# Kernel tuning notes

Hardware: AMD Instinct MI355X
Metric: run time of the kernel (lower is better)

## Reference

```python
import jax, jax.numpy as jnp
import numpy as np

B, DIM_IN, DIM_OUT = 2048, 4096, 4096


def setup_inputs() -> dict:
    key = jax.random.key(0)
    k1, k2, k3 = jax.random.split(key, 3)
    # binary input activations (0/1), stored as int32
    x = jax.random.randint(k1, (B, DIM_IN), 0, 2, dtype=jnp.int32)
    masks = jax.random.uniform(k2, (DIM_IN, DIM_OUT)) < 0.5
    # integer thresholds in [0, dim_in)
    thresholds = jax.random.randint(k3, (DIM_OUT,), 0, DIM_IN, dtype=jnp.int32)
    return {"x": x, "masks": masks, "thresholds": thresholds}


def reference(x, masks, thresholds):
    # Original: expand x to (B, dim_in, dim_out), XNOR with masks, sum over dim_in,
    # compare vs thresholds. XNOR(a,b) = a*b + (1-a)*(1-b), so the sum over dim_in
    # is two GEMMs -- never materialize the (B, dim_in, dim_out) tensor.
    xf = x.astype(jnp.float32)              # (B, dim_in), values in {0,1}
    mf = masks.astype(jnp.float32)          # (dim_in, dim_out)
    sums = xf @ mf + (1.0 - xf) @ (1.0 - mf)  # (B, dim_out), popcount of agreements
    return sums > thresholds.astype(jnp.float32)[None, :]  # (B, dim_out) bool
```

## Files before the change

### kernel.cpp

```cpp
#include <hip/hip_runtime.h>
#include <stdint.h>

#define BB    2048
#define DIN   4096
#define DOUT  4096


using v4i  = __attribute__((ext_vector_type(4)))  int;
using v16i = __attribute__((ext_vector_type(16))) int;

__device__ __forceinline__ void async_load16(const void* g, void* l) {
    __builtin_amdgcn_global_load_lds(
        (const __attribute__((address_space(1))) unsigned int*)g,
        (__attribute__((address_space(3))) unsigned int*)l,
        16, 0, 0);
}

__device__ __forceinline__ unsigned int to_pm1(unsigned int c) {
    return c + ((c ^ 0x01010101u) * 255u);
}

__global__ void pack_all(const int* __restrict__ x,
                         const void* __restrict__ mraw,
                         char* __restrict__ x8,
                         char* __restrict__ m8T) {
    const int tid = threadIdx.x;
    if (blockIdx.x < BB) {
        const int row = blockIdx.x;
        const int4* src = (const int4*)(x + (size_t)row * DIN);
        unsigned int* dst = (unsigned int*)(x8 + (size_t)row * DIN);
        #pragma unroll
        for (int q = 0; q < 4; ++q) {
            int4 v = src[q * 256 + tid];
            unsigned int t = (unsigned int)(v.x & 1) |
                             ((unsigned int)(v.y & 1) << 8) |
                             ((unsigned int)(v.z & 1) << 16) |
                             ((unsigned int)(v.w & 1) << 24);
            dst[q * 256 + tid] = to_pm1(t);
        }
    } else {
        const int bw = blockIdx.x - BB;
        const int n0 = (bw >> 4) * 64;
        const int k0 = (bw & 15) * 256;

        __shared__ unsigned int tl[64][68];

        const unsigned char* mb = (const unsigned char*)mraw;
        const unsigned int pv = *(const unsigned int*)(mb + (tid & 63) * 4);
        const bool isU8 = __any(pv > 1u);

        const int kq4  = tid >> 2;
        const int nq16 = (tid & 3) * 16;
        unsigned int b[4][4];
        if (isU8) {
            #pragma unroll
            for (int r = 0; r < 4; ++r) {
                uint4 v = *(const uint4*)(mb + (size_t)(k0 + kq4 * 4 + r) * DOUT
                                          + n0 + nq16);
                b[r][0] = v.x; b[r][1] = v.y; b[r][2] = v.z; b[r][3] = v.w;
            }
        } else {
            const int4* m32 = (const int4*)mraw;
            #pragma unroll
            for (int r = 0; r < 4; ++r)
                #pragma unroll
                for (int q = 0; q < 4; ++q) {
                    int4 v = m32[((size_t)(k0 + kq4 * 4 + r) * DOUT
                                  + n0 + nq16 + q * 4) >> 2];
                    b[r][q] = (unsigned int)(v.x & 1) |
                              ((unsigned int)(v.y & 1) << 8) |
                              ((unsigned int)(v.z & 1) << 16) |
                              ((unsigned int)(v.w & 1) << 24);
                }
        }
        #pragma unroll
        for (int w = 0; w < 4; ++w) {
            unsigned int a0 = b[0][w], a1 = b[1][w], a2 = b[2][w], a3 = b[3][w];
            unsigned int x0 = __builtin_amdgcn_perm(a1, a0, 0x05010400u);
            unsigned int x1 = __builtin_amdgcn_perm(a3, a2, 0x05010400u);
            unsigned int x2 = __builtin_amdgcn_perm(a1, a0, 0x07030602u);
            unsigned int x3 = __builtin_amdgcn_perm(a3, a2, 0x07030602u);
            unsigned int c0 = __builtin_amdgcn_perm(x1, x0, 0x05040100u);
            unsigned int c1 = __builtin_amdgcn_perm(x1, x0, 0x07060302u);
            unsigned int c2 = __builtin_amdgcn_perm(x3, x2, 0x05040100u);
            unsigned int c3 = __builtin_amdgcn_perm(x3, x2, 0x07060302u);
            tl[nq16 + w * 4 + 0][kq4] = to_pm1(c0);
            tl[nq16 + w * 4 + 1][kq4] = to_pm1(c1);
            tl[nq16 + w * 4 + 2][kq4] = to_pm1(c2);
            tl[nq16 + w * 4 + 3][kq4] = to_pm1(c3);
        }
        __syncthreads();

        const int nr = tid >> 2;
        const int c4 = tid & 3;
        #pragma unroll
        for (int q = 0; q < 4; ++q) {
            uint4 v = *(const uint4*)&tl[nr][4 * (c4 + 4 * q)];
            *(uint4*)(m8T + (size_t)(n0 + nr) * DIN + k0 + 16 * (c4 + 4 * q)) = v;
        }
    }
}

__global__ __launch_bounds__(512)
void bgemm(const char* __restrict__ x8,
           const char* __restrict__ m8T,
           const int* __restrict__ thr,
           int* __restrict__ out) {
    const int flat = blockIdx.x;
    const int xcd  = flat & 7;
    const int idx  = flat >> 3;
    const int bm   = (xcd & 1) * 4 + (idx & 3);
    const int bn   = (xcd >> 1) * 8 + (idx >> 2);
    const int b0   = bm * 256;
    const int o0   = bn * 128;

    const int tid  = threadIdx.x;
    const int lane = tid & 63;
    const int wv   = tid >> 6;
    const int im   = wv & 1;
    const int in_  = (wv >> 1) & 1;
    const int kh   = wv >> 2;
    const int wm   = im * 128;
    const int wn   = in_ * 64;
    const int l31  = lane & 31;
    const int lh   = lane >> 5;
    const int rsw  = l31 & 7;

    __shared__ __align__(16) char lds[3 * 49152];

    auto stage = [&](int c, int buf) {
        char* bufA = lds + buf * 49152;
        char* bufB = bufA + 32768;
        const int k0 = c * 128;
        const int r8 = lane >> 3;
        const int sl = lane & 7;
        #pragma unroll
        for (int h = 0; h < 4; ++h) {
            const int r0  = wv * 32 + h * 8;
            const int row = r0 + r8;
            const int g   = sl ^ (row & 7);
            async_load16(x8 + (size_t)(b0 + row) * DIN + k0 + g * 16,
                         bufA + r0 * 128 + lane * 16);
        }
        #pragma unroll
        for (int h = 0; h < 2; ++h) {
            const int r0  = wv * 16 + h * 8;
            const int row = r0 + r8;
            const int g   = sl ^ (row & 7);
            async_load16(m8T + (size_t)(o0 + row) * DIN + k0 + g * 16,
                         bufB + r0 * 128 + lane * 16);
        }
    };

    v16i acc[4][2];
    #pragma unroll
    for (int t = 0; t < 4; ++t)
        #pragma unroll
        for (int u = 0; u < 2; ++u)
            acc[t][u] = (v16i)(0);

    stage(0, 0);
    stage(1, 1);

    for (int c = 0; c < 32; ++c) {
        if (c < 31) asm volatile("s_waitcnt vmcnt(6)" ::: "memory");
        else        asm volatile("s_waitcnt vmcnt(0)" ::: "memory");
        __builtin_amdgcn_s_barrier();
        if (c < 30) stage(c + 2, (c + 2) % 3);

        const char* bufA = lds + (c % 3) * 49152;
        const char* bufB = bufA + 32768;
        #pragma unroll
        for (int ks = 0; ks < 2; ++ks) {
            const int slot = (((kh * 4 + ks * 2 + lh) ^ rsw)) * 16;
            v4i aF[4], bF[2];
            #pragma unroll
            for (int t = 0; t < 4; ++t)
                aF[t] = *(const v4i*)&bufA[(wm + t * 32 + l31) * 128 + slot];
            #pragma unroll
            for (int u = 0; u < 2; ++u)
                bF[u] = *(const v4i*)&bufB[(wn + u * 32 + l31) * 128 + slot];
            #pragma unroll
            for (int t = 0; t < 4; ++t)
                #pragma unroll
                for (int u = 0; u < 2; ++u)
                    acc[t][u] = __builtin_amdgcn_mfma_i32_32x32x32_i8(
                        aF[t], bF[u], acc[t][u], 0, 0, 0);
        }
    }
    __syncthreads();

    int* pool = (int*)lds;
    const int p = wv & 3;
    {
        const int give0 = kh ? 0 : 2;
        const int bw_ = p * 8192 + (kh ? 0 : 1) * 4096;
        #pragma unroll
        for (int tt = 0; tt < 2; ++tt) {
            const int t = give0 + tt;
            #pragma unroll
            for (int u = 0; u < 2; ++u)
                #pragma unroll
                for (int r = 0; r < 16; ++r) {
                    const int rowl = (r & 3) + 8 * (r >> 2) + 4 * lh;
                    pool[bw_ + (tt * 32 + rowl) * 64 + u * 32 + l31] = acc[t][u][r];
                }
        }
    }
    __syncthreads();
    const int keep0 = kh ? 2 : 0;
    const int br_ = p * 8192 + kh * 4096;
    #pragma unroll
    for (int tt = 0; tt < 2; ++tt) {
        const int t = keep0 + tt;
        #pragma unroll
        for (int u = 0; u < 2; ++u)
            #pragma unroll
            for (int r = 0; r < 16; ++r) {
                const int rowl = (r & 3) + 8 * (r >> 2) + 4 * lh;
                acc[t][u][r] += pool[br_ + (tt * 32 + rowl) * 64 + u * 32 + l31];
            }
    }

    #pragma unroll
    for (int u = 0; u < 2; ++u) {
        const int o   = o0 + wn + u * 32 + l31;
        const int lim = 2 * thr[o] - DIN;
        #pragma unroll
        for (int tt = 0; tt < 2; ++tt) {
            const int t = keep0 + tt;
            #pragma unroll
            for (int r = 0; r < 16; ++r) {
                const int rowl = (r & 3) + 8 * (r >> 2) + 4 * lh;
                const int b    = b0 + wm + kh * 64 + tt * 32 + rowl;
                out[(size_t)b * DOUT + o] = (acc[t][u][r] > lim) ? 1 : 0;
            }
        }
    }
}

extern "C" void kernel_launch(void* const* d_in, const int* in_sizes, int n_in,
                              void* d_out, int out_size, void* d_ws, size_t ws_size,
                              hipStream_t stream) {
    const int* x          = (const int*)d_in[0];
    const void* masks     = d_in[1];
    const int* thresholds = (const int*)d_in[2];
    int* out              = (int*)d_out;

    char* x8  = (char*)d_ws;
    char* m8T = (char*)d_ws + ((size_t)8 << 20);

    pack_all<<<BB + 1024, 256, 0, stream>>>(x, masks, x8, m8T);
    bgemm<<<256, 512, 0, stream>>>(x8, m8T, thresholds, out);
}
```

Before: 174.0 us.

## Pack operands into MFMA fragment-major layout for contiguous loads

The pack kernel now writes x and the transposed mask directly in a fragment-tiled layout: 32 rows by 32 k-bytes, each 1 KB block ordered the way a lane reads it. The GEMM stage loads each 1 KB fragment as one contiguous wave-wide async copy. LDS reads become lane*16 offsets with no XOR swizzle. This is meant to make global loads fully coalesced and to remove swizzle address math and LDS bank conflicts. The pack-side writes become more scattered, and the linear LDS reads may bring back bank conflicts.

```diff
diff --git a/kernel.cpp b/kernel.cpp
--- a/kernel.cpp
+++ b/kernel.cpp
@@ -22,13 +22,14 @@
 
 __global__ void pack_all(const int* __restrict__ x,
                          const void* __restrict__ mraw,
-                         char* __restrict__ x8,
-                         char* __restrict__ m8T) {
+                         char* __restrict__ x8f,
+                         char* __restrict__ m8Tf) {
     const int tid = threadIdx.x;
     if (blockIdx.x < BB) {
         const int row = blockIdx.x;
+        const int rb  = row >> 5;
+        const int rl  = row & 31;
         const int4* src = (const int4*)(x + (size_t)row * DIN);
-        unsigned int* dst = (unsigned int*)(x8 + (size_t)row * DIN);
         #pragma unroll
         for (int q = 0; q < 4; ++q) {
             int4 v = src[q * 256 + tid];
@@ -36,7 +37,10 @@
                              ((unsigned int)(v.y & 1) << 8) |
                              ((unsigned int)(v.z & 1) << 16) |
                              ((unsigned int)(v.w & 1) << 24);
-            dst[q * 256 + tid] = to_pm1(t);
+            const int w   = q * 256 + tid;
+            const int off = rb * 131072 + (w >> 3) * 1024 +
+                            (rl + 32 * ((w >> 2) & 1)) * 16 + 4 * (w & 3);
+            *(unsigned int*)(x8f + off) = to_pm1(t);
         }
     } else {
         const int bw = blockIdx.x - BB;
@@ -91,19 +95,25 @@
         }
         __syncthreads();
 
-        const int nr = tid >> 2;
-        const int c4 = tid & 3;
-        #pragma unroll
-        for (int q = 0; q < 4; ++q) {
-            uint4 v = *(const uint4*)&tl[nr][4 * (c4 + 4 * q)];
-            *(uint4*)(m8T + (size_t)(n0 + nr) * DIN + k0 + 16 * (c4 + 4 * q)) = v;
+        const int l  = tid & 63;
+        const int wvp = tid >> 6;
+        #pragma unroll
+        for (int j = 0; j < 4; ++j) {
+            const int idxc = wvp * 4 + j;
+            const int nbl  = idxc >> 3;
+            const int kpl  = idxc & 7;
+            uint4 v = *(const uint4*)&tl[nbl * 32 + (l & 31)]
+                                       [kpl * 8 + (l >> 5) * 4];
+            const size_t off = (size_t)((n0 >> 5) + nbl) * 131072 +
+                               (size_t)((k0 >> 5) + kpl) * 1024 + l * 16;
+            *(uint4*)(m8Tf + off) = v;
         }
     }
 }
 
 __global__ __launch_bounds__(512)
-void bgemm(const char* __restrict__ x8,
-           const char* __restrict__ m8T,
+void bgemm(const char* __restrict__ x8f,
+           const char* __restrict__ m8Tf,
            const int* __restrict__ thr,
            int* __restrict__ out) {
     const int flat = blockIdx.x;
@@ -124,31 +134,28 @@
     const int wn   = in_ * 64;
     const int l31  = lane & 31;
     const int lh   = lane >> 5;
-    const int rsw  = l31 & 7;
 
     __shared__ __align__(16) char lds[3 * 49152];
 
     auto stage = [&](int c, int buf) {
         char* bufA = lds + buf * 49152;
         char* bufB = bufA + 32768;
-        const int k0 = c * 128;
-        const int r8 = lane >> 3;
-        const int sl = lane & 7;
-        #pragma unroll
-        for (int h = 0; h < 4; ++h) {
-            const int r0  = wv * 32 + h * 8;
-            const int row = r0 + r8;
-            const int g   = sl ^ (row & 7);
-            async_load16(x8 + (size_t)(b0 + row) * DIN + k0 + g * 16,
-                         bufA + r0 * 128 + lane * 16);
-        }
-        #pragma unroll
-        for (int h = 0; h < 2; ++h) {
-            const int r0  = wv * 16 + h * 8;
-            const int row = r0 + r8;
-            const int g   = sl ^ (row & 7);
-            async_load16(m8T + (size_t)(o0 + row) * DIN + k0 + g * 16,
-                         bufB + r0 * 128 + lane * 16);
+        const int kp0 = c * 4;
+        #pragma unroll
+        for (int j = 0; j < 4; ++j) {
+            const int ci = wv * 4 + j;
+            const int rb = ci >> 2, kp = ci & 3;
+            async_load16(x8f + (size_t)(bm * 8 + rb) * 131072 +
+                               (size_t)(kp0 + kp) * 1024 + lane * 16,
+                         bufA + ci * 1024 + lane * 16);
+        }
+        #pragma unroll
+        for (int j = 0; j < 2; ++j) {
+            const int ci = wv * 2 + j;
+            const int nb = ci >> 2, kp = ci & 3;
+            async_load16(m8Tf + (size_t)(bn * 4 + nb) * 131072 +
+                                (size_t)(kp0 + kp) * 1024 + lane * 16,
+                         bufB + ci * 1024 + lane * 16);
         }
     };
 
@@ -172,14 +179,16 @@
         const char* bufB = bufA + 32768;
         #pragma unroll
         for (int ks = 0; ks < 2; ++ks) {
-            const int slot = (((kh * 4 + ks * 2 + lh) ^ rsw)) * 16;
+            const int kp = kh * 2 + ks;
             v4i aF[4], bF[2];
             #pragma unroll
             for (int t = 0; t < 4; ++t)
-                aF[t] = *(const v4i*)&bufA[(wm + t * 32 + l31) * 128 + slot];
+                aF[t] = *(const v4i*)&bufA[((im * 4 + t) * 4 + kp) * 1024
+                                           + lane * 16];
             #pragma unroll
             for (int u = 0; u < 2; ++u)
-                bF[u] = *(const v4i*)&bufB[(wn + u * 32 + l31) * 128 + slot];
+                bF[u] = *(const v4i*)&bufB[((in_ * 2 + u) * 4 + kp) * 1024
+                                           + lane * 16];
             #pragma unroll
             for (int t = 0; t < 4; ++t)
                 #pragma unroll
@@ -247,9 +256,9 @@
     const int* thresholds = (const int*)d_in[2];
     int* out              = (int*)d_out;
 
-    char* x8  = (char*)d_ws;
-    char* m8T = (char*)d_ws + ((size_t)8 << 20);
-
-    pack_all<<<BB + 1024, 256, 0, stream>>>(x, masks, x8, m8T);
-    bgemm<<<256, 512, 0, stream>>>(x8, m8T, thresholds, out);
-}
+    char* x8f  = (char*)d_ws;
+    char* m8Tf = (char*)d_ws + ((size_t)8 << 20);
+
+    pack_all<<<BB + 1024, 256, 0, stream>>>(x, masks, x8f, m8Tf);
+    bgemm<<<256, 512, 0, stream>>>(x8f, m8Tf, thresholds, out);
+}
```

Measured after the change: 175.7 us. No clear change (+1.0%).
